# Kernel optimization log

Hardware: AMD Instinct MI355X
Metric: run time of the kernel (lower is better)

## Reference

```python
import jax, jax.numpy as jnp
import numpy as np

N_NODES = 50000
N_EDGES = 800000
D_FEAT = 128
UNITS = 256
K = 3


def setup_inputs() -> dict:
    key = jax.random.key(0)
    k1, k2, k3, k4 = jax.random.split(key, 4)
    x = jax.random.normal(k1, (N_NODES, D_FEAT), dtype=jnp.float32)
    edge_index = jax.random.randint(k2, (2, N_EDGES), 0, N_NODES, dtype=jnp.int32)
    edge_weight = jnp.ones((N_EDGES,), dtype=jnp.float32)
    # glorot-uniform kernel [(K+1)*D, UNITS], zero bias
    fan_in, fan_out = D_FEAT * (K + 1), UNITS
    limit = np.sqrt(6.0 / (fan_in + fan_out)).astype(np.float32)
    kernel = jax.random.uniform(k3, (fan_in, fan_out), minval=-limit, maxval=limit, dtype=jnp.float32)
    bias = jnp.zeros((UNITS,), dtype=jnp.float32)
    return {"x": x, "edge_index": edge_index, "edge_weight": edge_weight,
            "kernel": kernel, "bias": bias}


def reference(x, edge_index, edge_weight, kernel, bias):
    n = x.shape[0]
    row, col = edge_index[0], edge_index[1]
    # symmetric GCN normalization (renorm=False: normalize first, then self-loops w=1)
    deg = jax.ops.segment_sum(edge_weight, row, num_segments=n)
    deg_inv_sqrt = jnp.where(deg > 0, jax.lax.rsqrt(jnp.where(deg > 0, deg, 1.0)), 0.0)
    normed_w = deg_inv_sqrt[row] * edge_weight * deg_inv_sqrt[col]
    loop = jnp.arange(n, dtype=row.dtype)
    row2 = jnp.concatenate([row, loop])
    col2 = jnp.concatenate([col, loop])
    w2 = jnp.concatenate([normed_w, jnp.ones((n,), dtype=normed_w.dtype)])
    # K-hop propagation, collecting each hop
    xs = [x]
    h = x
    for _ in range(K):
        msg = h[col2] * w2[:, None]            # [E+N, D] gather + scale
        h = jax.ops.segment_sum(msg, row2, num_segments=n)  # scatter-sum
        xs.append(h)
    hcat = jnp.concatenate(xs, axis=-1)        # [N, (K+1)*D]
    out = hcat @ kernel + bias
    return jax.nn.relu(out)
```

## Files before the change

### kernel.cpp

```cpp
#include <hip/hip_runtime.h>

#define NN 50000
#define NP 50048
#define NE 800000
#define D 128
#define UNITS 256
#define KTOT 512
#define SCAN_NB 196
#define NREP 16
#define CONV_NB 6250
#define COUNT_NB 3125

typedef __attribute__((ext_vector_type(8))) short short8;
typedef __attribute__((ext_vector_type(4))) float floatx4;

__device__ inline unsigned short f2b(float f) {
    unsigned u = __float_as_uint(f);
    return (unsigned short)((u + 0x7fff + ((u >> 16) & 1)) >> 16);
}
__device__ inline float2 bx2f(unsigned v) {
    float2 r;
    r.x = __uint_as_float(v << 16);
    r.y = __uint_as_float(v & 0xffff0000u);
    return r;
}

__global__ __launch_bounds__(256) void count_prep_kernel(const int* __restrict__ row,
                                                         int* __restrict__ cnt16,
                                                         int* __restrict__ rank,
                                                         const float* __restrict__ x,
                                                         unsigned* __restrict__ xb,
                                                         const float* __restrict__ W,
                                                         short* __restrict__ Wt) {
    __shared__ float tile[32][33];
    int b = blockIdx.x;
    if (b < COUNT_NB) {
        int e = b * 256 + threadIdx.x;
        if (e < NE) {
            int r = row[e];
            int rep = (e >> 6) & (NREP - 1);
            rank[e] = atomicAdd(&cnt16[rep * NN + r], 1);
        }
    } else if (b < COUNT_NB + CONV_NB) {
        int t = (b - COUNT_NB) * 256 + threadIdx.x;
        float4 v = ((const float4*)x)[t];
        uint2 o;
        o.x = (unsigned)f2b(v.x) | ((unsigned)f2b(v.y) << 16);
        o.y = (unsigned)f2b(v.z) | ((unsigned)f2b(v.w) << 16);
        ((uint2*)xb)[t] = o;
    } else {
        int bb = b - COUNT_NB - CONV_NB;
        int kb = (bb & 15) * 32;
        int nb = (bb >> 4) * 32;
        int tx = threadIdx.x & 31, ty = threadIdx.x >> 5;
        for (int i = 0; i < 32; i += 8)
            tile[ty + i][tx] = W[(size_t)(kb + ty + i) * UNITS + nb + tx];
        __syncthreads();
        for (int i = 0; i < 32; i += 8)
            Wt[(size_t)(nb + ty + i) * KTOT + kb + tx] = (short)f2b(tile[tx][ty + i]);
    }
}

__global__ __launch_bounds__(256) void scanA_kernel(int* __restrict__ cnt16,
                                                    int* __restrict__ row_ptr,
                                                    int* __restrict__ bsum) {
    __shared__ int s[256];
    int t = threadIdx.x;
    int idx = blockIdx.x * 256 + t;
    int tot = 0;
    if (idx < NN) {
        int c[NREP];
#pragma unroll
        for (int r = 0; r < NREP; ++r) c[r] = cnt16[r * NN + idx];
        int run = 0;
#pragma unroll
        for (int r = 0; r < NREP; ++r) {
            cnt16[r * NN + idx] = run;
            run += c[r];
        }
        tot = run;
    }
    s[t] = tot;
    __syncthreads();
    for (int off = 1; off < 256; off <<= 1) {
        int add = (t >= off) ? s[t - off] : 0;
        __syncthreads();
        s[t] += add;
        __syncthreads();
    }
    if (idx < NN) row_ptr[idx] = s[t] - tot;
    if (t == 255) bsum[blockIdx.x] = s[255];
}

__global__ __launch_bounds__(256) void scanC_kernel(int* __restrict__ row_ptr,
                                                    const int* __restrict__ bsum) {
    __shared__ int soff_s;
    int b = blockIdx.x, t = threadIdx.x;
    if (t < 64) {
        int acc = 0;
        for (int i = t; i < b; i += 64) acc += bsum[i];
#pragma unroll
        for (int off = 32; off; off >>= 1) acc += __shfl_down(acc, off);
        if (t == 0) soff_s = acc;
    }
    __syncthreads();
    int idx = b * 256 + t;
    if (idx < NN) row_ptr[idx] += soff_s;
    if (b == 0 && t == 0) row_ptr[NN] = NE;
}

__global__ void fill_kernel(const int* __restrict__ row, const int* __restrict__ col,
                            const float* __restrict__ w, const int* __restrict__ rank,
                            const int* __restrict__ row_ptr, const int* __restrict__ cnt16,
                            int2* __restrict__ edges, int E) {
    int e = blockIdx.x * blockDim.x + threadIdx.x;
    if (e >= E) return;
    int r = row[e];
    int rep = (e >> 6) & (NREP - 1);
    int pos = row_ptr[r] + cnt16[rep * NN + r] + rank[e];
    edges[pos] = make_int2(col[e], __float_as_int(w[e]));
}

__global__ __launch_bounds__(256) void degdis_kernel(const int* __restrict__ row_ptr,
                                                     const int2* __restrict__ edges,
                                                     float* __restrict__ dis) {
    int node = blockIdx.x * 4 + (threadIdx.x >> 6);
    int l = threadIdx.x & 63;
    if (node >= NN) return;
    int beg = row_ptr[node], end = row_ptr[node + 1];
    float s = 0.f;
    for (int e = beg + l; e < end; e += 64) s += __int_as_float(edges[e].y);
#pragma unroll
    for (int off = 32; off; off >>= 1) s += __shfl_down(s, off);
    if (l == 0) dis[node] = s > 0.f ? rsqrtf(s) : 0.f;
}

__device__ inline void acc8(float* acc, uint4 v, float w) {
    float2 f0 = bx2f(v.x), f1 = bx2f(v.y), f2 = bx2f(v.z), f3 = bx2f(v.w);
    acc[0] = fmaf(w, f0.x, acc[0]); acc[1] = fmaf(w, f0.y, acc[1]);
    acc[2] = fmaf(w, f1.x, acc[2]); acc[3] = fmaf(w, f1.y, acc[3]);
    acc[4] = fmaf(w, f2.x, acc[4]); acc[5] = fmaf(w, f2.y, acc[5]);
    acc[6] = fmaf(w, f3.x, acc[6]); acc[7] = fmaf(w, f3.y, acc[7]);
}

template <bool NORM>
__global__ __launch_bounds__(256) void gather_kernel(const unsigned* __restrict__ hprev,
                                                     unsigned* __restrict__ hnext,
                                                     const int* __restrict__ row_ptr,
                                                     int2* __restrict__ edges,
                                                     const float* __restrict__ dis) {
    int node = blockIdx.x * 4 + (threadIdx.x >> 6);
    if (node >= NN) return;
    int l = threadIdx.x & 63;
    int g = l >> 4;
    int s = l & 15;
    const uint4* hp4 = (const uint4*)hprev;
    int beg = row_ptr[node], end = row_ptr[node + 1];
    float dr = NORM ? dis[node] : 1.f;
    int last = (end - 1 > beg) ? end - 1 : beg;
    if (last >= NE) last = NE - 1;

    float acc[8] = {0.f, 0.f, 0.f, 0.f, 0.f, 0.f, 0.f, 0.f};
    int2 M[4];
#pragma unroll
    for (int b = 0; b < 4; ++b) {
        int i = beg + b * 4 + g;
        M[b] = edges[i < end ? i : last];
    }
    for (int e = beg; e < end; e += 16) {
        int2 E[4];
#pragma unroll
        for (int b = 0; b < 4; ++b) E[b] = M[b];
        int en = e + 16;
        if (en < end) {
#pragma unroll
            for (int b = 0; b < 4; ++b) {
                int j = en + b * 4 + g;
                M[b] = edges[j < end ? j : last];
            }
        }
        float wgt[4];
        uint4 v[4];
#pragma unroll
        for (int b = 0; b < 4; ++b) {
            float wv = __int_as_float(E[b].y);
            if (NORM) wv *= dr * dis[E[b].x];
            int i = e + b * 4 + g;
            wgt[b] = (i < end) ? wv : 0.f;
            v[b] = hp4[(size_t)E[b].x * 16 + s];
        }
#pragma unroll
        for (int b = 0; b < 4; ++b) acc8(acc, v[b], wgt[b]);
        if (NORM && s == 0) {
#pragma unroll
            for (int b = 0; b < 4; ++b) {
                int i = e + b * 4 + g;
                if (i < end) edges[i].y = __float_as_int(wgt[b]);
            }
        }
    }
#pragma unroll
    for (int i = 0; i < 8; ++i) {
        acc[i] += __shfl_xor(acc[i], 16);
        acc[i] += __shfl_xor(acc[i], 32);
    }
    if (g == 0) {
        uint4 sv = hp4[(size_t)node * 16 + s];
        acc8(acc, sv, 1.f);
        uint4 o;
        o.x = (unsigned)f2b(acc[0]) | ((unsigned)f2b(acc[1]) << 16);
        o.y = (unsigned)f2b(acc[2]) | ((unsigned)f2b(acc[3]) << 16);
        o.z = (unsigned)f2b(acc[4]) | ((unsigned)f2b(acc[5]) << 16);
        o.w = (unsigned)f2b(acc[6]) | ((unsigned)f2b(acc[7]) << 16);
        ((uint4*)hnext)[(size_t)node * 16 + s] = o;
    }
}

#define BK 32
#define NIT (KTOT / BK)
#define GLDS(g, l)                                                                      \
    __builtin_amdgcn_global_load_lds((const __attribute__((address_space(1))) void*)(g), \
                                     (__attribute__((address_space(3))) void*)(l), 16, 0, 0)

__global__ __launch_bounds__(256) void gemm_mfma(const short* __restrict__ A0,
                                                 const short* __restrict__ Wt,
                                                 const float* __restrict__ bias,
                                                 float* __restrict__ C) {
    __shared__ short As[2][64 * BK];
    __shared__ short Bs[2][128 * BK];
    const int t = threadIdx.x;
    const int m0 = blockIdx.x * 64;
    const int n0 = blockIdx.y * 128;
    const int w = t >> 6;
    const int l = t & 63;
    const int wr = (w >> 1) * 32;
    const int wc = (w & 1) * 64;
    const int lm = l & 15;
    const int lg = l >> 4;
    const int srow = l >> 2;
    const int soff = ((l & 3) ^ ((l >> 3) & 3)) * 8;

    floatx4 zero = {0.f, 0.f, 0.f, 0.f};
    floatx4 acc[2][4];
#pragma unroll
    for (int r = 0; r < 2; ++r)
#pragma unroll
        for (int c = 0; c < 4; ++c) acc[r][c] = zero;

#define STAGE(IT, BUF)                                                                  \
    do {                                                                                \
        int kk = (IT) * BK;                                                             \
        const short* Asrc = A0 + (size_t)(kk >> 7) * ((size_t)NP * 128) + (kk & 127);   \
        const short* Bsrc = Wt + kk;                                                    \
        GLDS(Asrc + (size_t)(m0 + w * 16 + srow) * D + soff, &As[BUF][w * 512]);        \
        GLDS(Bsrc + (size_t)(n0 + (2 * w) * 16 + srow) * KTOT + soff,                   \
             &Bs[BUF][(2 * w) * 512]);                                                  \
        GLDS(Bsrc + (size_t)(n0 + (2 * w + 1) * 16 + srow) * KTOT + soff,               \
             &Bs[BUF][(2 * w + 1) * 512]);                                              \
    } while (0)

    STAGE(0, 0);
    __syncthreads();
    for (int it = 0; it < NIT; ++it) {
        int cur = it & 1;
        if (it + 1 < NIT) STAGE(it + 1, cur ^ 1);
        short8 af[2], bf[4];
#pragma unroll
        for (int r = 0; r < 2; ++r) {
            int rowv = wr + r * 16 + lm;
            int p = lg ^ ((rowv >> 1) & 3);
            af[r] = *(const short8*)&As[cur][rowv * BK + p * 8];
        }
#pragma unroll
        for (int c = 0; c < 4; ++c) {
            int rowv = wc + c * 16 + lm;
            int p = lg ^ ((rowv >> 1) & 3);
            bf[c] = *(const short8*)&Bs[cur][rowv * BK + p * 8];
        }
#pragma unroll
        for (int r = 0; r < 2; ++r)
#pragma unroll
            for (int c = 0; c < 4; ++c)
                acc[r][c] = __builtin_amdgcn_mfma_f32_16x16x32_bf16(af[r], bf[c],
                                                                    acc[r][c], 0, 0, 0);
        __syncthreads();
    }
#undef STAGE

    const int q4 = lg * 4;
#pragma unroll
    for (int r = 0; r < 2; ++r) {
#pragma unroll
        for (int i = 0; i < 4; ++i) {
            int m = m0 + wr + r * 16 + q4 + i;
            if (m < NN) {
#pragma unroll
                for (int c = 0; c < 4; ++c) {
                    int n = n0 + wc + c * 16 + lm;
                    float v = acc[r][c][i] + bias[n];
                    C[(size_t)m * UNITS + n] = fmaxf(v, 0.f);
                }
            }
        }
    }
}

extern "C" void kernel_launch(void* const* d_in, const int* in_sizes, int n_in,
                              void* d_out, int out_size, void* d_ws, size_t ws_size,
                              hipStream_t stream) {
    const float* x = (const float*)d_in[0];
    const int* ei = (const int*)d_in[1];
    const float* ew_in = (const float*)d_in[2];
    const float* W = (const float*)d_in[3];
    const float* bias = (const float*)d_in[4];
    float* out = (float*)d_out;

    const int* row = ei;
    const int* col = ei + NE;

    float* dis = (float*)d_ws;
    int* cnt16 = (int*)(dis + NN);
    int* rank = cnt16 + NREP * NN;
    int* bsum = rank + NE;
    int* row_ptr = bsum + 256;
    int2* edges = (int2*)(row_ptr + NN + 2);
    unsigned* xb = (unsigned*)(((uintptr_t)(edges + NE) + 15) & ~(uintptr_t)15);
    unsigned* h1b = xb + (size_t)NP * 64;
    unsigned* h2b = h1b + (size_t)NP * 64;
    unsigned* h3b = h2b + (size_t)NP * 64;
    short* Wt = (short*)(h3b + (size_t)NP * 64);

    hipMemsetAsync(cnt16, 0, NREP * NN * sizeof(int), stream);

    count_prep_kernel<<<COUNT_NB + CONV_NB + 128, 256, 0, stream>>>(row, cnt16, rank,
                                                                    x, xb, W, Wt);
    scanA_kernel<<<SCAN_NB, 256, 0, stream>>>(cnt16, row_ptr, bsum);
    scanC_kernel<<<SCAN_NB, 256, 0, stream>>>(row_ptr, bsum);
    fill_kernel<<<(NE + 255) / 256, 256, 0, stream>>>(row, col, ew_in, rank, row_ptr, cnt16,
                                                      edges, NE);
    degdis_kernel<<<(NN + 3) / 4, 256, 0, stream>>>(row_ptr, edges, dis);

    int gat_blocks = (NN + 3) / 4;
    gather_kernel<true><<<gat_blocks, 256, 0, stream>>>(xb, h1b, row_ptr, edges, dis);
    gather_kernel<false><<<gat_blocks, 256, 0, stream>>>(h1b, h2b, row_ptr, edges, dis);
    gather_kernel<false><<<gat_blocks, 256, 0, stream>>>(h2b, h3b, row_ptr, edges, dis);

    gemm_mfma<<<dim3(NP / 64, UNITS / 128), 256, 0, stream>>>(
        (const short*)xb, Wt, bias, out);
}
```

Baseline: 315.6 us.

## Replace LDS-staged GEMM with register-direct MFMA loads and full-width wave tiles

The GEMM no longer stages A and B through LDS with global_load_lds and barriers. Each wave now loads its MFMA fragments straight from global memory into registers, double-buffered across K steps, and one block covers all 256 output columns with 64 rows per wave. A new extra block in the prep kernel zeroes the padded rows of the bf16 feature buffers, because the GEMM now reads those rows without any guard. This removes the LDS traffic and the synchronisation, at the cost of more register pressure, uncoalesced 16-byte global reads, and duplicate A reads across the four waves, which rely on the cache.

```diff
diff --git a/kernel.cpp b/kernel.cpp
--- a/kernel.cpp
+++ b/kernel.cpp
@@ -48,7 +48,7 @@
         o.x = (unsigned)f2b(v.x) | ((unsigned)f2b(v.y) << 16);
         o.y = (unsigned)f2b(v.z) | ((unsigned)f2b(v.w) << 16);
         ((uint2*)xb)[t] = o;
-    } else {
+    } else if (b < COUNT_NB + CONV_NB + 128) {
         int bb = b - COUNT_NB - CONV_NB;
         int kb = (bb & 15) * 32;
         int nb = (bb >> 4) * 32;
@@ -58,6 +58,15 @@
         __syncthreads();
         for (int i = 0; i < 32; i += 8)
             Wt[(size_t)(nb + ty + i) * KTOT + kb + tx] = (short)f2b(tile[tx][ty + i]);
+    } else {
+        uint4 z = {0u, 0u, 0u, 0u};
+        uint4* x4 = (uint4*)xb;
+        for (int i = threadIdx.x; i < 4 * 48 * 16; i += 256) {
+            int chunk = i / (48 * 16);
+            int rem = i - chunk * (48 * 16);
+            int rowp = NN + (rem >> 4);
+            x4[((size_t)chunk * NP + rowp) * 16 + (rem & 15)] = z;
+        }
     }
 }
 
@@ -216,87 +225,62 @@
     }
 }
 
-#define BK 32
-#define NIT (KTOT / BK)
-#define GLDS(g, l)                                                                      \
-    __builtin_amdgcn_global_load_lds((const __attribute__((address_space(1))) void*)(g), \
-                                     (__attribute__((address_space(3))) void*)(l), 16, 0, 0)
-
-__global__ __launch_bounds__(256) void gemm_mfma(const short* __restrict__ A0,
-                                                 const short* __restrict__ Wt,
-                                                 const float* __restrict__ bias,
-                                                 float* __restrict__ C) {
-    __shared__ short As[2][64 * BK];
-    __shared__ short Bs[2][128 * BK];
+#define LOADAB(AF, BF, KK)                                                                  \
+    do {                                                                                    \
+        const short* ap = A0 + (size_t)((KK) >> 7) * ((size_t)NP * 128) + ((KK) & 127);     \
+        _Pragma("unroll") for (int r = 0; r < 4; ++r)                                       \
+            AF[r] = *(const short8*)&ap[(size_t)(m0 + r * 16 + lm) * 128 + lg * 8];         \
+        _Pragma("unroll") for (int c = 0; c < 4; ++c)                                       \
+            BF[c] = *(const short8*)&Wt[(size_t)(n0 + c * 16 + lm) * KTOT + (KK) + lg * 8]; \
+    } while (0)
+
+#define MM(AF, BF)                                                                          \
+    do {                                                                                    \
+        _Pragma("unroll") for (int r = 0; r < 4; ++r)                                       \
+        _Pragma("unroll") for (int c = 0; c < 4; ++c)                                       \
+            acc[r][c] = __builtin_amdgcn_mfma_f32_16x16x32_bf16(AF[r], BF[c],               \
+                                                                acc[r][c], 0, 0, 0);        \
+    } while (0)
+
+__global__ __launch_bounds__(256, 2) void gemm_mfma(const short* __restrict__ A0,
+                                                    const short* __restrict__ Wt,
+                                                    const float* __restrict__ bias,
+                                                    float* __restrict__ C) {
     const int t = threadIdx.x;
     const int m0 = blockIdx.x * 64;
-    const int n0 = blockIdx.y * 128;
     const int w = t >> 6;
     const int l = t & 63;
-    const int wr = (w >> 1) * 32;
-    const int wc = (w & 1) * 64;
     const int lm = l & 15;
     const int lg = l >> 4;
-    const int srow = l >> 2;
-    const int soff = ((l & 3) ^ ((l >> 3) & 3)) * 8;
+    const int n0 = w * 64;
 
     floatx4 zero = {0.f, 0.f, 0.f, 0.f};
-    floatx4 acc[2][4];
-#pragma unroll
-    for (int r = 0; r < 2; ++r)
+    floatx4 acc[4][4];
+#pragma unroll
+    for (int r = 0; r < 4; ++r)
 #pragma unroll
         for (int c = 0; c < 4; ++c) acc[r][c] = zero;
 
-#define STAGE(IT, BUF)                                                                  \
-    do {                                                                                \
-        int kk = (IT) * BK;                                                             \
-        const short* Asrc = A0 + (size_t)(kk >> 7) * ((size_t)NP * 128) + (kk & 127);   \
-        const short* Bsrc = Wt + kk;                                                    \
-        GLDS(Asrc + (size_t)(m0 + w * 16 + srow) * D + soff, &As[BUF][w * 512]);        \
-        GLDS(Bsrc + (size_t)(n0 + (2 * w) * 16 + srow) * KTOT + soff,                   \
-             &Bs[BUF][(2 * w) * 512]);                                                  \
-        GLDS(Bsrc + (size_t)(n0 + (2 * w + 1) * 16 + srow) * KTOT + soff,               \
-             &Bs[BUF][(2 * w + 1) * 512]);                                              \
-    } while (0)
-
-    STAGE(0, 0);
-    __syncthreads();
-    for (int it = 0; it < NIT; ++it) {
-        int cur = it & 1;
-        if (it + 1 < NIT) STAGE(it + 1, cur ^ 1);
-        short8 af[2], bf[4];
-#pragma unroll
-        for (int r = 0; r < 2; ++r) {
-            int rowv = wr + r * 16 + lm;
-            int p = lg ^ ((rowv >> 1) & 3);
-            af[r] = *(const short8*)&As[cur][rowv * BK + p * 8];
-        }
-#pragma unroll
-        for (int c = 0; c < 4; ++c) {
-            int rowv = wc + c * 16 + lm;
-            int p = lg ^ ((rowv >> 1) & 3);
-            bf[c] = *(const short8*)&Bs[cur][rowv * BK + p * 8];
-        }
-#pragma unroll
-        for (int r = 0; r < 2; ++r)
-#pragma unroll
-            for (int c = 0; c < 4; ++c)
-                acc[r][c] = __builtin_amdgcn_mfma_f32_16x16x32_bf16(af[r], bf[c],
-                                                                    acc[r][c], 0, 0, 0);
-        __syncthreads();
-    }
-#undef STAGE
+    short8 a0[4], b0[4], a1[4], b1[4];
+    LOADAB(a0, b0, 0);
+#pragma unroll
+    for (int i = 0; i < 8; ++i) {
+        LOADAB(a1, b1, i * 64 + 32);
+        MM(a0, b0);
+        if (i < 7) LOADAB(a0, b0, i * 64 + 64);
+        MM(a1, b1);
+    }
 
     const int q4 = lg * 4;
 #pragma unroll
-    for (int r = 0; r < 2; ++r) {
+    for (int r = 0; r < 4; ++r) {
 #pragma unroll
         for (int i = 0; i < 4; ++i) {
-            int m = m0 + wr + r * 16 + q4 + i;
+            int m = m0 + r * 16 + q4 + i;
             if (m < NN) {
 #pragma unroll
                 for (int c = 0; c < 4; ++c) {
-                    int n = n0 + wc + c * 16 + lm;
+                    int n = n0 + c * 16 + lm;
                     float v = acc[r][c][i] + bias[n];
                     C[(size_t)m * UNITS + n] = fmaxf(v, 0.f);
                 }
@@ -332,8 +316,8 @@
 
     hipMemsetAsync(cnt16, 0, NREP * NN * sizeof(int), stream);
 
-    count_prep_kernel<<<COUNT_NB + CONV_NB + 128, 256, 0, stream>>>(row, cnt16, rank,
-                                                                    x, xb, W, Wt);
+    count_prep_kernel<<<COUNT_NB + CONV_NB + 128 + 1, 256, 0, stream>>>(row, cnt16, rank,
+                                                                        x, xb, W, Wt);
     scanA_kernel<<<SCAN_NB, 256, 0, stream>>>(cnt16, row_ptr, bsum);
     scanC_kernel<<<SCAN_NB, 256, 0, stream>>>(row_ptr, bsum);
     fill_kernel<<<(NE + 255) / 256, 256, 0, stream>>>(row, col, ew_in, rank, row_ptr, cnt16,
@@ -345,6 +329,5 @@
     gather_kernel<false><<<gat_blocks, 256, 0, stream>>>(h1b, h2b, row_ptr, edges, dis);
     gather_kernel<false><<<gat_blocks, 256, 0, stream>>>(h2b, h3b, row_ptr, edges, dis);
 
-    gemm_mfma<<<dim3(NP / 64, UNITS / 128), 256, 0, stream>>>(
-        (const short*)xb, Wt, bias, out);
-}
+    gemm_mfma<<<NP / 64, 256, 0, stream>>>((const short*)xb, Wt, bias, out);
+}
```

Result: slower. 332.2 us (+5.3%).

## Enlarge GEMM tile to 128x128 with XCD-aware block remap and waitcnt pipelining

Applied to the files above, without the earlier changes.

The final GEMM tile grows from 64x128 to 128x128 per workgroup, so each wave computes 4x4 MFMA tiles, which raises operand reuse out of LDS. The 1D grid is remapped so consecutive logical tiles land on the same XCD, and explicit vmcnt waits plus raw barriers replace __syncthreads so loads overlap with compute. An extra prep block zeroes the padded rows of the bf16 feature buffers, since the larger tile now reads past NN. In exchange the kernel uses more registers and LDS per block, and fewer blocks are launched.

```diff
diff --git a/kernel.cpp b/kernel.cpp
--- a/kernel.cpp
+++ b/kernel.cpp
@@ -48,7 +48,7 @@
         o.x = (unsigned)f2b(v.x) | ((unsigned)f2b(v.y) << 16);
         o.y = (unsigned)f2b(v.z) | ((unsigned)f2b(v.w) << 16);
         ((uint2*)xb)[t] = o;
-    } else {
+    } else if (b < COUNT_NB + CONV_NB + 128) {
         int bb = b - COUNT_NB - CONV_NB;
         int kb = (bb & 15) * 32;
         int nb = (bb >> 4) * 32;
@@ -58,6 +58,15 @@
         __syncthreads();
         for (int i = 0; i < 32; i += 8)
             Wt[(size_t)(nb + ty + i) * KTOT + kb + tx] = (short)f2b(tile[tx][ty + i]);
+    } else {
+        uint4 z = {0u, 0u, 0u, 0u};
+        uint4* x4 = (uint4*)xb;
+        for (int i = threadIdx.x; i < 4 * 48 * 16; i += 256) {
+            int chunk = i / (48 * 16);
+            int rem = i - chunk * (48 * 16);
+            int rowp = NN + (rem >> 4);
+            x4[((size_t)chunk * NP + rowp) * 16 + (rem & 15)] = z;
+        }
     }
 }
 
@@ -222,82 +231,97 @@
     __builtin_amdgcn_global_load_lds((const __attribute__((address_space(1))) void*)(g), \
                                      (__attribute__((address_space(3))) void*)(l), 16, 0, 0)
 
-__global__ __launch_bounds__(256) void gemm_mfma(const short* __restrict__ A0,
-                                                 const short* __restrict__ Wt,
-                                                 const float* __restrict__ bias,
-                                                 float* __restrict__ C) {
-    __shared__ short As[2][64 * BK];
+__global__ __launch_bounds__(256, 2) void gemm_mfma(const short* __restrict__ A0,
+                                                    const short* __restrict__ Wt,
+                                                    const float* __restrict__ bias,
+                                                    float* __restrict__ C) {
+    __shared__ short As[2][128 * BK];
     __shared__ short Bs[2][128 * BK];
+    const int nwg = 782;
+    int orig = blockIdx.x;
+    int xcd = orig & 7;
+    int q = nwg >> 3, r = nwg & 7;
+    int wgid = (xcd < r ? xcd * (q + 1) : r * (q + 1) + (xcd - r) * q) + (orig >> 3);
+    const int m0 = (wgid >> 1) * 128;
+    const int n0 = (wgid & 1) * 128;
+
     const int t = threadIdx.x;
-    const int m0 = blockIdx.x * 64;
-    const int n0 = blockIdx.y * 128;
     const int w = t >> 6;
     const int l = t & 63;
-    const int wr = (w >> 1) * 32;
+    const int wr = (w >> 1) * 64;
     const int wc = (w & 1) * 64;
     const int lm = l & 15;
     const int lg = l >> 4;
     const int srow = l >> 2;
-    const int soff = ((l & 3) ^ ((l >> 3) & 3)) * 8;
+    const int sc = ((l & 3) ^ ((l >> 3) & 3)) * 8;
 
     floatx4 zero = {0.f, 0.f, 0.f, 0.f};
-    floatx4 acc[2][4];
-#pragma unroll
-    for (int r = 0; r < 2; ++r)
-#pragma unroll
-        for (int c = 0; c < 4; ++c) acc[r][c] = zero;
+    floatx4 acc[4][4];
+#pragma unroll
+    for (int rr = 0; rr < 4; ++rr)
+#pragma unroll
+        for (int cc = 0; cc < 4; ++cc) acc[rr][cc] = zero;
 
 #define STAGE(IT, BUF)                                                                  \
     do {                                                                                \
         int kk = (IT) * BK;                                                             \
         const short* Asrc = A0 + (size_t)(kk >> 7) * ((size_t)NP * 128) + (kk & 127);   \
         const short* Bsrc = Wt + kk;                                                    \
-        GLDS(Asrc + (size_t)(m0 + w * 16 + srow) * D + soff, &As[BUF][w * 512]);        \
-        GLDS(Bsrc + (size_t)(n0 + (2 * w) * 16 + srow) * KTOT + soff,                   \
-             &Bs[BUF][(2 * w) * 512]);                                                  \
-        GLDS(Bsrc + (size_t)(n0 + (2 * w + 1) * 16 + srow) * KTOT + soff,               \
-             &Bs[BUF][(2 * w + 1) * 512]);                                              \
+        GLDS(Asrc + (size_t)(m0 + w * 32 + srow) * D + sc, &As[BUF][(w * 32) * 32 + l * 8]); \
+        GLDS(Asrc + (size_t)(m0 + w * 32 + 16 + srow) * D + sc,                         \
+             &As[BUF][(w * 32 + 16) * 32 + l * 8]);                                     \
+        GLDS(Bsrc + (size_t)(n0 + w * 32 + srow) * KTOT + sc,                           \
+             &Bs[BUF][(w * 32) * 32 + l * 8]);                                          \
+        GLDS(Bsrc + (size_t)(n0 + w * 32 + 16 + srow) * KTOT + sc,                      \
+             &Bs[BUF][(w * 32 + 16) * 32 + l * 8]);                                     \
     } while (0)
 
     STAGE(0, 0);
-    __syncthreads();
     for (int it = 0; it < NIT; ++it) {
         int cur = it & 1;
-        if (it + 1 < NIT) STAGE(it + 1, cur ^ 1);
-        short8 af[2], bf[4];
-#pragma unroll
-        for (int r = 0; r < 2; ++r) {
-            int rowv = wr + r * 16 + lm;
+        if (it + 1 < NIT) {
+            STAGE(it + 1, cur ^ 1);
+            asm volatile("s_waitcnt vmcnt(4)" ::: "memory");
+        } else {
+            asm volatile("s_waitcnt vmcnt(0)" ::: "memory");
+        }
+        __builtin_amdgcn_s_barrier();
+        __builtin_amdgcn_sched_barrier(0);
+        short8 af[4], bf[4];
+#pragma unroll
+        for (int rr = 0; rr < 4; ++rr) {
+            int rowv = wr + rr * 16 + lm;
             int p = lg ^ ((rowv >> 1) & 3);
-            af[r] = *(const short8*)&As[cur][rowv * BK + p * 8];
-        }
-#pragma unroll
-        for (int c = 0; c < 4; ++c) {
-            int rowv = wc + c * 16 + lm;
+            af[rr] = *(const short8*)&As[cur][rowv * BK + p * 8];
+        }
+#pragma unroll
+        for (int cc = 0; cc < 4; ++cc) {
+            int rowv = wc + cc * 16 + lm;
             int p = lg ^ ((rowv >> 1) & 3);
-            bf[c] = *(const short8*)&Bs[cur][rowv * BK + p * 8];
-        }
-#pragma unroll
-        for (int r = 0; r < 2; ++r)
-#pragma unroll
-            for (int c = 0; c < 4; ++c)
-                acc[r][c] = __builtin_amdgcn_mfma_f32_16x16x32_bf16(af[r], bf[c],
-                                                                    acc[r][c], 0, 0, 0);
-        __syncthreads();
+            bf[cc] = *(const short8*)&Bs[cur][rowv * BK + p * 8];
+        }
+#pragma unroll
+        for (int rr = 0; rr < 4; ++rr)
+#pragma unroll
+            for (int cc = 0; cc < 4; ++cc)
+                acc[rr][cc] = __builtin_amdgcn_mfma_f32_16x16x32_bf16(af[rr], bf[cc],
+                                                                      acc[rr][cc], 0, 0, 0);
+        __builtin_amdgcn_sched_barrier(0);
+        __builtin_amdgcn_s_barrier();
     }
 #undef STAGE
 
     const int q4 = lg * 4;
 #pragma unroll
-    for (int r = 0; r < 2; ++r) {
+    for (int rr = 0; rr < 4; ++rr) {
 #pragma unroll
         for (int i = 0; i < 4; ++i) {
-            int m = m0 + wr + r * 16 + q4 + i;
+            int m = m0 + wr + rr * 16 + q4 + i;
             if (m < NN) {
 #pragma unroll
-                for (int c = 0; c < 4; ++c) {
-                    int n = n0 + wc + c * 16 + lm;
-                    float v = acc[r][c][i] + bias[n];
+                for (int cc = 0; cc < 4; ++cc) {
+                    int n = n0 + wc + cc * 16 + lm;
+                    float v = acc[rr][cc][i] + bias[n];
                     C[(size_t)m * UNITS + n] = fmaxf(v, 0.f);
                 }
             }
@@ -332,8 +356,8 @@
 
     hipMemsetAsync(cnt16, 0, NREP * NN * sizeof(int), stream);
 
-    count_prep_kernel<<<COUNT_NB + CONV_NB + 128, 256, 0, stream>>>(row, cnt16, rank,
-                                                                    x, xb, W, Wt);
+    count_prep_kernel<<<COUNT_NB + CONV_NB + 128 + 1, 256, 0, stream>>>(row, cnt16, rank,
+                                                                        x, xb, W, Wt);
     scanA_kernel<<<SCAN_NB, 256, 0, stream>>>(cnt16, row_ptr, bsum);
     scanC_kernel<<<SCAN_NB, 256, 0, stream>>>(row_ptr, bsum);
     fill_kernel<<<(NE + 255) / 256, 256, 0, stream>>>(row, col, ew_in, rank, row_ptr, cnt16,
@@ -345,6 +369,5 @@
     gather_kernel<false><<<gat_blocks, 256, 0, stream>>>(h1b, h2b, row_ptr, edges, dis);
     gather_kernel<false><<<gat_blocks, 256, 0, stream>>>(h2b, h3b, row_ptr, edges, dis);
 
-    gemm_mfma<<<dim3(NP / 64, UNITS / 128), 256, 0, stream>>>(
-        (const short*)xb, Wt, bias, out);
-}
+    gemm_mfma<<<782, 256, 0, stream>>>((const short*)xb, Wt, bias, out);
+}
```

After: 300.0 us (median of 2 runs). -5.0%, faster.
